# Kernel tuning notes

Measured on AMD Instinct MI355X. Metric: run time of the kernel, lower is better.

The kernel has to match this reference:

```python
import jax, jax.numpy as jnp
import numpy as np

TEMPERATURE = 8.0  # sqrt(d_k=64)

def setup_inputs() -> dict:
    key = jax.random.key(0)
    kq, kk, kv, km1, km2 = jax.random.split(key, 5)
    B, Lq, Lk, D = 128, 512, 512, 64
    q = jax.random.normal(kq, (B, Lq, D), dtype=jnp.float32)
    k = jax.random.normal(kk, (B, Lk, D), dtype=jnp.float32)
    v = jax.random.normal(kv, (B, Lk, D), dtype=jnp.float32)
    key_mask = jax.random.bernoulli(km1, 0.5, (B, Lq, Lk))
    query_mask = jax.random.bernoulli(km2, 0.5, (B, Lq, Lk))
    return {"q": q, "k": k, "v": v, "key_mask": key_mask, "query_mask": query_mask}

def reference(q, k, v, key_mask, query_mask):
    # attn = (q @ k^T) / temperature, pre-softmax key masking with -inf
    scores = jnp.einsum('bqd,bkd->bqk', q, k) / TEMPERATURE
    scores = jnp.where(key_mask, -jnp.inf, scores)
    attn = jax.nn.softmax(scores, axis=-1)
    # post-softmax query-row zeroing
    attn = jnp.where(query_mask, 0.0, attn)
    # dropout omitted (eval mode / deterministic reference)
    output = jnp.einsum('bqk,bkd->bqd', attn, v)
    return (output, attn)
```

## Files before the change

kernel.cpp:

```cpp
#include <hip/hip_runtime.h>
#include <hip/hip_bf16.h>

#define BATCH 128
#define LQ    512
#define LK    512
#define DH    64
#define TQ    16
#define KC    128

#define SSTR  520
#define VROW  136

typedef float    float4v __attribute__((ext_vector_type(4)));
typedef short    short8v __attribute__((ext_vector_type(8)));
typedef short    short4v __attribute__((ext_vector_type(4)));
typedef int      int4v   __attribute__((ext_vector_type(4)));
typedef _Float16 half4v  __attribute__((ext_vector_type(4)));

__device__ __forceinline__ short bf16r(float f) {
  union { float f; unsigned u; } x; x.f = f;
  unsigned r = x.u + 0x7FFFu + ((x.u >> 16) & 1u);
  return (short)(r >> 16);
}

__device__ __forceinline__ int4v ntload4(const int* p) {
  return __builtin_nontemporal_load((const int4v*)p);
}

__device__ __forceinline__ void loadVchunk(const float* __restrict__ vsrc,
                                           int tid, float4v vr[8]) {
#pragma unroll
  for (int it = 0; it < 2; ++it) {
    int Bx = tid + 256 * it;
    int bR = Bx >> 4, bC = Bx & 15;
    const float* vp = vsrc + bR * 4 * DH + bC * 4;
#pragma unroll
    for (int r = 0; r < 4; ++r)
      vr[it * 4 + r] = *(const float4v*)(vp + r * DH);
  }
}

__device__ __forceinline__ void storeVchunk(short* vt, int tid,
                                            const float4v vr[8]) {
#pragma unroll
  for (int it = 0; it < 2; ++it) {
    int Bx = tid + 256 * it;
    int bR = Bx >> 4, bC = Bx & 15;
#pragma unroll
    for (int e = 0; e < 4; ++e) {
      int d  = bC * 4 + e;
      int gp = bR ^ (d & 31);
      short4v s4;
      s4[0] = bf16r(vr[it * 4 + 0][e]); s4[1] = bf16r(vr[it * 4 + 1][e]);
      s4[2] = bf16r(vr[it * 4 + 2][e]); s4[3] = bf16r(vr[it * 4 + 3][e]);
      *(short4v*)&vt[d * VROW + gp * 4] = s4;
    }
  }
}

__global__ __launch_bounds__(256, 4)
void sdpa_kernel(const float* __restrict__ Q, const float* __restrict__ K,
                 const float* __restrict__ V, const int* __restrict__ KM,
                 const int* __restrict__ QM, float* __restrict__ OUT,
                 float* __restrict__ ATT)
{
  __shared__ short scs[TQ * SSTR];
  __shared__ short vt[DH * VROW];

  const int b    = blockIdx.x >> 5;
  const int q0   = (blockIdx.x & 31) * TQ;
  const int tid  = threadIdx.x;
  const int lane = tid & 63;
  const int wave = tid >> 6;
  const int lm   = lane & 15;
  const int quad = lane >> 4;

  const int row = tid >> 4;
  const int col = tid & 15;
  const size_t gro = (size_t)(b * LQ + q0 + row) * LK;

  int4v kmv[8];
#pragma unroll
  for (int j = 0; j < 8; ++j)
    kmv[j] = ntload4(KM + gro + col * 4 + j * 64);

  const float* qrow = Q + ((size_t)(b * LQ + q0 + lm)) * DH + quad * 8;
  short8v aq0, aq1;
  {
    float4v f0 = __builtin_nontemporal_load((const float4v*)(qrow + 0));
    float4v f1 = __builtin_nontemporal_load((const float4v*)(qrow + 4));
    float4v f2 = __builtin_nontemporal_load((const float4v*)(qrow + 32));
    float4v f3 = __builtin_nontemporal_load((const float4v*)(qrow + 36));
#pragma unroll
    for (int e = 0; e < 4; ++e) {
      aq0[e]     = bf16r(f0[e]);
      aq0[e + 4] = bf16r(f1[e]);
      aq1[e]     = bf16r(f2[e]);
      aq1[e + 4] = bf16r(f3[e]);
    }
  }

  {
    float4v c0, c1, c2, c3;
    {
      const float* kr = K + ((size_t)(b * LK + (wave * 2) * 16 + lm)) * DH + quad * 8;
      c0 = *(const float4v*)(kr + 0);  c1 = *(const float4v*)(kr + 4);
      c2 = *(const float4v*)(kr + 32); c3 = *(const float4v*)(kr + 36);
    }
#pragma unroll
    for (int p = 0; p < 8; ++p) {
      float4v n0, n1, n2, n3;
      if (p < 7) {
        int np = p + 1, kt = np >> 1, t = np & 1;
        const float* kr = K + ((size_t)(b * LK + kt * KC + (wave * 2 + t) * 16 + lm)) * DH + quad * 8;
        n0 = *(const float4v*)(kr + 0);  n1 = *(const float4v*)(kr + 4);
        n2 = *(const float4v*)(kr + 32); n3 = *(const float4v*)(kr + 36);
      }
      short8v b0, b1;
#pragma unroll
      for (int e = 0; e < 4; ++e) {
        b0[e]     = bf16r(c0[e]);
        b0[e + 4] = bf16r(c1[e]);
        b1[e]     = bf16r(c2[e]);
        b1[e + 4] = bf16r(c3[e]);
      }
      float4v acc = {0.f, 0.f, 0.f, 0.f};
      acc = __builtin_amdgcn_mfma_f32_16x16x32_bf16(aq0, b0, acc, 0, 0, 0);
      acc = __builtin_amdgcn_mfma_f32_16x16x32_bf16(aq1, b1, acc, 0, 0, 0);
      int kt = p >> 1, t = p & 1;
      int n  = kt * KC + (wave * 2 + t) * 16 + lm;
      int m0 = quad * 4;
#pragma unroll
      for (int j = 0; j < 4; ++j)
        *(_Float16*)&scs[(m0 + j) * SSTR + n] = (_Float16)acc[j];
      if (p < 7) { c0 = n0; c1 = n1; c2 = n2; c3 = n3; }
    }
  }
  __syncthreads();

  float s[32];
  float mx = -INFINITY;
#pragma unroll
  for (int j = 0; j < 8; ++j) {
    half4v h4 = *(const half4v*)&scs[row * SSTR + col * 4 + j * 64];
#pragma unroll
    for (int e = 0; e < 4; ++e) {
      float val = kmv[j][e] ? -INFINITY : (float)h4[e];
      s[j * 4 + e] = val;
      mx = fmaxf(mx, val);
    }
  }
  int4v qmv[8];
#pragma unroll
  for (int j = 0; j < 8; ++j)
    qmv[j] = ntload4(QM + gro + col * 4 + j * 64);
  float4v vr[8];
  loadVchunk(V + ((size_t)(b * LK)) * DH, tid, vr);

#pragma unroll
  for (int off = 8; off; off >>= 1) mx = fmaxf(mx, __shfl_xor(mx, off, 64));
  float sum = 0.f;
#pragma unroll
  for (int j = 0; j < 32; ++j) {
    float p = __expf((s[j] - mx) * 0.125f);
    s[j] = p;
    sum += p;
  }
#pragma unroll
  for (int off = 8; off; off >>= 1) sum += __shfl_xor(sum, off, 64);
  const float inv = 1.f / sum;
  float* arow = ATT + gro;
#pragma unroll
  for (int j = 0; j < 8; ++j) {
    int kk = col * 4 + j * 64;
    float4v a4;
#pragma unroll
    for (int e = 0; e < 4; ++e)
      a4[e] = qmv[j][e] ? 0.f : s[j * 4 + e] * inv;
    __builtin_nontemporal_store(a4, (float4v*)(arow + kk));
    short4v ab;
    ab[0] = bf16r(a4[0]); ab[1] = bf16r(a4[1]);
    ab[2] = bf16r(a4[2]); ab[3] = bf16r(a4[3]);
    *(short4v*)&scs[row * SSTR + kk] = ab;
  }
  storeVchunk(vt, tid, vr);
  __syncthreads();

  float4v oacc = {0.f, 0.f, 0.f, 0.f};
#pragma unroll
  for (int kt = 0; kt < 4; ++kt) {
    if (kt < 3)
      loadVchunk(V + ((size_t)(b * LK + (kt + 1) * KC)) * DH, tid, vr);
#pragma unroll
    for (int ks = 0; ks < 4; ++ks) {
      const short* ap = &scs[lm * SSTR + kt * KC + ks * 32 + quad * 8];
      short8v a8 = *(const short8v*)ap;
      int n  = wave * 16 + lm;
      int g0 = ks * 8 + quad * 2;
      short4v lo = *(const short4v*)&vt[n * VROW + ((g0    ) ^ (n & 31)) * 4];
      short4v hi = *(const short4v*)&vt[n * VROW + ((g0 + 1) ^ (n & 31)) * 4];
      short8v b8;
      b8[0] = lo[0]; b8[1] = lo[1]; b8[2] = lo[2]; b8[3] = lo[3];
      b8[4] = hi[0]; b8[5] = hi[1]; b8[6] = hi[2]; b8[7] = hi[3];
      oacc = __builtin_amdgcn_mfma_f32_16x16x32_bf16(a8, b8, oacc, 0, 0, 0);
    }
    if (kt < 3) {
      __syncthreads();
      storeVchunk(vt, tid, vr);
      __syncthreads();
    }
  }
  {
    int m0 = quad * 4;
    float* obase = OUT + ((size_t)(b * LQ + q0 + m0)) * DH + wave * 16 + lm;
#pragma unroll
    for (int j = 0; j < 4; ++j)
      __builtin_nontemporal_store(oacc[j], obase + j * DH);
  }
}

extern "C" void kernel_launch(void* const* d_in, const int* in_sizes, int n_in,
                              void* d_out, int out_size, void* d_ws, size_t ws_size,
                              hipStream_t stream) {
  const float* q  = (const float*)d_in[0];
  const float* k  = (const float*)d_in[1];
  const float* v  = (const float*)d_in[2];
  const int*   km = (const int*)d_in[3];
  const int*   qm = (const int*)d_in[4];
  float* out  = (float*)d_out;
  float* attn = out + (size_t)BATCH * LQ * DH;
  dim3 grid(BATCH * (LQ / TQ));
  dim3 block(256);
  hipLaunchKernelGGL(sdpa_kernel, grid, block, 0, stream,
                     q, k, v, km, qm, out, attn);
}
```

Before: 388.4 us.

## Stage V per-wave in LDS to drop block barriers; use packed bf16 conversion

The V staging for the PV product is restructured so that each wave loads and transposes only the 16 output columns it consumes into a private LDS slice, in 64-row chunks. This removes the block-wide __syncthreads pairs between V chunks and shrinks the LDS footprint, which allows the occupancy hint to go from 4 to 6 blocks per CU. The scalar bf16 rounding is also replaced by a packed conversion builtin where one is available. The cost is that each wave now issues its own V loads, and there are more, smaller chunk iterations with less cooperative loading.

Result: slower. 419.0 us (+7.9%).

```diff
diff --git a/kernel.cpp b/kernel.cpp
--- a/kernel.cpp
+++ b/kernel.cpp
@@ -7,9 +7,10 @@
 #define DH    64
 #define TQ    16
 #define KC    128
+#define VC    64
 
 #define SSTR  520
-#define VROW  136
+
 
 typedef float    float4v __attribute__((ext_vector_type(4)));
 typedef short    short8v __attribute__((ext_vector_type(8)));
@@ -23,49 +24,28 @@
   return (short)(r >> 16);
 }
 
+__device__ __forceinline__ unsigned pkbf16(float a, float b) {
+#if __has_builtin(__builtin_amdgcn_cvt_pk_bf16_f32)
+  auto r = __builtin_amdgcn_cvt_pk_bf16_f32(a, b);
+  unsigned i; __builtin_memcpy(&i, &r, 4); return i;
+#else
+  return ((unsigned)(unsigned short)bf16r(a)) |
+         ((unsigned)(unsigned short)bf16r(b) << 16);
+#endif
+}
+
 __device__ __forceinline__ int4v ntload4(const int* p) {
   return __builtin_nontemporal_load((const int4v*)p);
 }
 
-__device__ __forceinline__ void loadVchunk(const float* __restrict__ vsrc,
-                                           int tid, float4v vr[8]) {
-#pragma unroll
-  for (int it = 0; it < 2; ++it) {
-    int Bx = tid + 256 * it;
-    int bR = Bx >> 4, bC = Bx & 15;
-    const float* vp = vsrc + bR * 4 * DH + bC * 4;
-#pragma unroll
-    for (int r = 0; r < 4; ++r)
-      vr[it * 4 + r] = *(const float4v*)(vp + r * DH);
-  }
-}
-
-__device__ __forceinline__ void storeVchunk(short* vt, int tid,
-                                            const float4v vr[8]) {
-#pragma unroll
-  for (int it = 0; it < 2; ++it) {
-    int Bx = tid + 256 * it;
-    int bR = Bx >> 4, bC = Bx & 15;
-#pragma unroll
-    for (int e = 0; e < 4; ++e) {
-      int d  = bC * 4 + e;
-      int gp = bR ^ (d & 31);
-      short4v s4;
-      s4[0] = bf16r(vr[it * 4 + 0][e]); s4[1] = bf16r(vr[it * 4 + 1][e]);
-      s4[2] = bf16r(vr[it * 4 + 2][e]); s4[3] = bf16r(vr[it * 4 + 3][e]);
-      *(short4v*)&vt[d * VROW + gp * 4] = s4;
-    }
-  }
-}
-
-__global__ __launch_bounds__(256, 4)
+__global__ __launch_bounds__(256, 6)
 void sdpa_kernel(const float* __restrict__ Q, const float* __restrict__ K,
                  const float* __restrict__ V, const int* __restrict__ KM,
                  const int* __restrict__ QM, float* __restrict__ OUT,
                  float* __restrict__ ATT)
 {
   __shared__ short scs[TQ * SSTR];
-  __shared__ short vt[DH * VROW];
+  __shared__ short vt[4 * 16 * VC];
 
   const int b    = blockIdx.x >> 5;
   const int q0   = (blockIdx.x & 31) * TQ;
@@ -91,13 +71,12 @@
     float4v f1 = __builtin_nontemporal_load((const float4v*)(qrow + 4));
     float4v f2 = __builtin_nontemporal_load((const float4v*)(qrow + 32));
     float4v f3 = __builtin_nontemporal_load((const float4v*)(qrow + 36));
-#pragma unroll
-    for (int e = 0; e < 4; ++e) {
-      aq0[e]     = bf16r(f0[e]);
-      aq0[e + 4] = bf16r(f1[e]);
-      aq1[e]     = bf16r(f2[e]);
-      aq1[e + 4] = bf16r(f3[e]);
-    }
+    unsigned* a0 = (unsigned*)&aq0;
+    unsigned* a1 = (unsigned*)&aq1;
+    a0[0] = pkbf16(f0[0], f0[1]); a0[1] = pkbf16(f0[2], f0[3]);
+    a0[2] = pkbf16(f1[0], f1[1]); a0[3] = pkbf16(f1[2], f1[3]);
+    a1[0] = pkbf16(f2[0], f2[1]); a1[1] = pkbf16(f2[2], f2[3]);
+    a1[2] = pkbf16(f3[0], f3[1]); a1[3] = pkbf16(f3[2], f3[3]);
   }
 
   {
@@ -117,12 +96,13 @@
         n2 = *(const float4v*)(kr + 32); n3 = *(const float4v*)(kr + 36);
       }
       short8v b0, b1;
-#pragma unroll
-      for (int e = 0; e < 4; ++e) {
-        b0[e]     = bf16r(c0[e]);
-        b0[e + 4] = bf16r(c1[e]);
-        b1[e]     = bf16r(c2[e]);
-        b1[e + 4] = bf16r(c3[e]);
+      {
+        unsigned* p0 = (unsigned*)&b0;
+        unsigned* p1 = (unsigned*)&b1;
+        p0[0] = pkbf16(c0[0], c0[1]); p0[1] = pkbf16(c0[2], c0[3]);
+        p0[2] = pkbf16(c1[0], c1[1]); p0[3] = pkbf16(c1[2], c1[3]);
+        p1[0] = pkbf16(c2[0], c2[1]); p1[1] = pkbf16(c2[2], c2[3]);
+        p1[2] = pkbf16(c3[0], c3[1]); p1[3] = pkbf16(c3[2], c3[3]);
       }
       float4v acc = {0.f, 0.f, 0.f, 0.f};
       acc = __builtin_amdgcn_mfma_f32_16x16x32_bf16(aq0, b0, acc, 0, 0, 0);
@@ -154,9 +134,6 @@
 #pragma unroll
   for (int j = 0; j < 8; ++j)
     qmv[j] = ntload4(QM + gro + col * 4 + j * 64);
-  float4v vr[8];
-  loadVchunk(V + ((size_t)(b * LK)) * DH, tid, vr);
-
 #pragma unroll
   for (int off = 8; off; off >>= 1) mx = fmaxf(mx, __shfl_xor(mx, off, 64));
   float sum = 0.f;
@@ -179,35 +156,57 @@
       a4[e] = qmv[j][e] ? 0.f : s[j * 4 + e] * inv;
     __builtin_nontemporal_store(a4, (float4v*)(arow + kk));
     short4v ab;
-    ab[0] = bf16r(a4[0]); ab[1] = bf16r(a4[1]);
-    ab[2] = bf16r(a4[2]); ab[3] = bf16r(a4[3]);
+    unsigned* abp = (unsigned*)&ab;
+    abp[0] = pkbf16(a4[0], a4[1]);
+    abp[1] = pkbf16(a4[2], a4[3]);
     *(short4v*)&scs[row * SSTR + kk] = ab;
   }
-  storeVchunk(vt, tid, vr);
+
+  const int Bk = lm;
+  short* vtw = vt + wave * (16 * VC);
+
+  float4v vr[4];
+  {
+    const float* vp = V + ((size_t)(b * LK + Bk * 4)) * DH + wave * 16 + quad * 4;
+#pragma unroll
+    for (int r = 0; r < 4; ++r) vr[r] = *(const float4v*)(vp + r * DH);
+  }
   __syncthreads();
 
   float4v oacc = {0.f, 0.f, 0.f, 0.f};
 #pragma unroll
-  for (int kt = 0; kt < 4; ++kt) {
-    if (kt < 3)
-      loadVchunk(V + ((size_t)(b * LK + (kt + 1) * KC)) * DH, tid, vr);
-#pragma unroll
-    for (int ks = 0; ks < 4; ++ks) {
-      const short* ap = &scs[lm * SSTR + kt * KC + ks * 32 + quad * 8];
+  for (int c = 0; c < 8; ++c) {
+    float4v vn[4];
+    if (c < 7) {
+      const float* vp = V + ((size_t)(b * LK + (c + 1) * VC + Bk * 4)) * DH + wave * 16 + quad * 4;
+#pragma unroll
+      for (int r = 0; r < 4; ++r) vn[r] = *(const float4v*)(vp + r * DH);
+    }
+#pragma unroll
+    for (int e = 0; e < 4; ++e) {
+      int dp = quad * 4 + e;
+      int gp = Bk ^ dp;
+      short4v s4;
+      unsigned* sp = (unsigned*)&s4;
+      sp[0] = pkbf16(vr[0][e], vr[1][e]);
+      sp[1] = pkbf16(vr[2][e], vr[3][e]);
+      *(short4v*)&vtw[dp * VC + gp * 4] = s4;
+    }
+#pragma unroll
+    for (int ks = 0; ks < 2; ++ks) {
+      const short* ap = &scs[lm * SSTR + c * VC + ks * 32 + quad * 8];
       short8v a8 = *(const short8v*)ap;
-      int n  = wave * 16 + lm;
       int g0 = ks * 8 + quad * 2;
-      short4v lo = *(const short4v*)&vt[n * VROW + ((g0    ) ^ (n & 31)) * 4];
-      short4v hi = *(const short4v*)&vt[n * VROW + ((g0 + 1) ^ (n & 31)) * 4];
+      short4v lo = *(const short4v*)&vtw[lm * VC + ((g0    ) ^ lm) * 4];
+      short4v hi = *(const short4v*)&vtw[lm * VC + ((g0 + 1) ^ lm) * 4];
       short8v b8;
       b8[0] = lo[0]; b8[1] = lo[1]; b8[2] = lo[2]; b8[3] = lo[3];
       b8[4] = hi[0]; b8[5] = hi[1]; b8[6] = hi[2]; b8[7] = hi[3];
       oacc = __builtin_amdgcn_mfma_f32_16x16x32_bf16(a8, b8, oacc, 0, 0, 0);
     }
-    if (kt < 3) {
-      __syncthreads();
-      storeVchunk(vt, tid, vr);
-      __syncthreads();
+    if (c < 7) {
+#pragma unroll
+      for (int r = 0; r < 4; ++r) vr[r] = vn[r];
     }
   }
   {
```
